# Optimization experiments

Hardware: AMD Instinct MI355X
Metric: run time of the kernel (lower is better)

## Reference

```python
import jax, jax.numpy as jnp
import numpy as np
from jax import lax

BN_EPS = 1e-5
B, C_IN, HW = 512, 3, 128  # crop batch, channels, crop size
C1, C2 = 32, 64
DIST_THRESHOLD = 0.55


def setup_inputs() -> dict:
    key = jax.random.key(0)
    ks = jax.random.split(key, 13)
    return {
        "crops": jax.random.normal(ks[0], (B, C_IN, HW, HW), jnp.float32),
        "w1": jax.random.normal(ks[1], (C1, C_IN, 3, 3), jnp.float32) * 0.1,
        "b1": jax.random.normal(ks[2], (C1,), jnp.float32) * 0.1,
        "g1": jax.random.uniform(ks[3], (C1,), jnp.float32),
        "be1": jax.random.normal(ks[4], (C1,), jnp.float32) * 0.1,
        "m1": jax.random.normal(ks[5], (C1,), jnp.float32) * 0.1,
        "v1": jax.random.uniform(ks[6], (C1,), jnp.float32),
        "w2": jax.random.normal(ks[7], (C2, C1, 3, 3), jnp.float32) * 0.05,
        "b2": jax.random.normal(ks[8], (C2,), jnp.float32) * 0.1,
        "g2": jax.random.uniform(ks[9], (C2,), jnp.float32),
        "be2": jax.random.normal(ks[10], (C2,), jnp.float32) * 0.1,
        "m2": jax.random.normal(ks[11], (C2,), jnp.float32) * 0.1,
        "v2": jax.random.uniform(ks[12], (C2,), jnp.float32),
    }


def _conv(x, w, b, stride):
    y = lax.conv_general_dilated(
        x, w, window_strides=(stride, stride), padding=((1, 1), (1, 1)),
        dimension_numbers=("NCHW", "OIHW", "NCHW"))
    return y + b[None, :, None, None]


def _bn(x, gamma, beta, mean, var):
    inv = gamma * lax.rsqrt(var + BN_EPS)
    return x * inv[None, :, None, None] + (beta - mean * inv)[None, :, None, None]


def _maxpool2(x):
    return lax.reduce_window(x, -jnp.inf, lax.max, (1, 1, 2, 2), (1, 1, 2, 2), "VALID")


def reference(crops, w1, b1, g1, be1, m1, v1, w2, b2, g2, be2, m2, v2):
    # layer1: Conv(3->32, s1, p1) + BN + ReLU + MaxPool2  -> [B, 32, 64, 64]
    h = _maxpool2(jax.nn.relu(_bn(_conv(crops, w1, b1, 1), g1, be1, m1, v1)))
    # layer2: Conv(32->64, s2, p1) + BN + Sigmoid + MaxPool2 -> [B, 64, 16, 16]
    feat = _maxpool2(jax.nn.sigmoid(_bn(_conv(h, w2, b2, 2), g2, be2, m2, v2)))
    # per-crop distribution score thresholded as in uniqueDistribution/MLE
    scores = feat.mean(axis=(1, 2, 3))            # [B]
    detected = scores >= DIST_THRESHOLD           # [B] bool
    return feat, scores, detected
```

## Files before the change

### kernel.cpp

```cpp
#include <hip/hip_runtime.h>
#include <math.h>

#define BN_EPS 1e-5f
#define HW_ 128

typedef unsigned short u16_t;
typedef unsigned int u32_t;

typedef __bf16 bf16x8 __attribute__((ext_vector_type(8)));
typedef float f32x4 __attribute__((ext_vector_type(4)));
typedef float f32x16 __attribute__((ext_vector_type(16)));
typedef u32_t u32x4 __attribute__((ext_vector_type(4)));
typedef u32x4 u32x4_ma __attribute__((may_alias));
typedef u16_t u16_ma __attribute__((may_alias));

static __device__ __forceinline__ u16_t f2bf(float f) {
    u32_t u = __float_as_uint(f);
    return (u16_t)((u + 0x7FFFu + ((u >> 16) & 1u)) >> 16);
}
static __device__ __forceinline__ u32_t packbf(float a, float b) {
    return (u32_t)f2bf(a) | ((u32_t)f2bf(b) << 16);
}
static __device__ __forceinline__ bf16x8 ld_frag16(const u16_t* p) {
    union { u32x4 u; bf16x8 f; } x;
    x.u = *(const u32x4_ma*)p;
    return x.f;
}
static __device__ __forceinline__ bf16x8 ld_frag32(const u32_t* p) {
    union { u32x4 u; bf16x8 f; } x;
    x.u = *(const u32x4_ma*)p;
    return x.f;
}
static __device__ __forceinline__ bf16x8 asbf(u32x4 u) {
    union { u32x4 u; bf16x8 f; } x;
    x.u = u;
    return x.f;
}

#define WSUM_OFF 0
#define W2R_OFF  512
#define WF_OFF   9728
#define PT_OFF   11008
#define BN1_OFF  12288
#define BN2_OFF  12352
#define WS_TOTAL 12480

#define CI_PITCH 304
#define CI_U32   (36 * 152)

__global__ __launch_bounds__(512) void prep_kernel(
    const float* __restrict__ w1, const float* __restrict__ b1,
    const float* __restrict__ g1, const float* __restrict__ be1,
    const float* __restrict__ m1, const float* __restrict__ v1,
    const float* __restrict__ w2, const float* __restrict__ b2,
    const float* __restrict__ g2, const float* __restrict__ be2,
    const float* __restrict__ m2, const float* __restrict__ v2,
    u32_t* __restrict__ ws)
{
    const int tid = threadIdx.x;
    ws[WSUM_OFF + tid] = 0u;

    for (int idx = tid; idx < 9216; idx += 512) {
        int H   = idx / 4608;
        int rem = idx - H * 4608;
        int tap = rem >> 9;
        int r2  = rem & 511;
        int ocl = r2 >> 4;
        int icp = r2 & 15;
        const float* wp = w2 + (H * 32 + ocl) * 288 + tap;
        ws[W2R_OFF + idx] = packbf(wp[(2 * icp) * 9], wp[(2 * icp + 1) * 9]);
    }
    if (tid < 320) {
        int s = tid >> 6, lane = tid & 63;
        int n32 = lane & 31, halfk = lane >> 5;
        int p = 2 * s + halfk;
        bool valid = (p <= 8);
        const float* wp = w1 + n32 * 27 + (valid ? p : 8);
        float wa = valid ? wp[0]  : 0.f;
        float wb = valid ? wp[9]  : 0.f;
        float wc = valid ? wp[18] : 0.f;
        u32x4 f;
        f[0] = packbf(wa, wb); f[1] = packbf(wc, 0.f); f[2] = 0u; f[3] = 0u;
        ((u32x4_ma*)(ws + WF_OFF))[tid] = f;
    }
    for (int idx = tid; idx < 1280; idx += 512) {
        int tt = idx >> 5, n32 = idx & 31;
        int gA = n32 >> 2, sub = n32 & 3;
        int pA = tt * 8 + gA;
        int gy = (pA * 241) >> 12; gy = min(gy, 16);
        int gx = min(pA - gy * 17, 16); gx = max(gx, 0);
        int cy = 2 * gy + (sub >> 1), cx = 2 * gx + (sub & 1);
        ws[PT_OFF + idx] = (u32_t)(cy * CI_PITCH + cx * 8);
    }
    if (tid < 32) {
        float inv = g1[tid] * rsqrtf(v1[tid] + BN_EPS);
        float sh  = b1[tid] * inv + be1[tid] - m1[tid] * inv;
        ws[BN1_OFF + 2 * tid]     = __float_as_uint(inv);
        ws[BN1_OFF + 2 * tid + 1] = __float_as_uint(sh);
    }
    if (tid >= 64 && tid < 128) {
        int ch = tid - 64;
        float inv = g2[ch] * rsqrtf(v2[ch] + BN_EPS);
        float sh  = b2[ch] * inv + be2[ch] - m2[ch] * inv;
        ws[BN2_OFF + 2 * ch]     = __float_as_uint(inv);
        ws[BN2_OFF + 2 * ch + 1] = __float_as_uint(sh);
    }
}

__global__ __launch_bounds__(512, 8) void fused_cnn_kernel(
    const float* __restrict__ crops, const u32_t* __restrict__ tab,
    float* __restrict__ out, float* __restrict__ wsum)
{
    __shared__ __align__(16) u32_t uniS[CI_U32];
    __shared__ __align__(16) u16_t hS[289 * 32];
    __shared__ float redS[8];

    const int tid  = threadIdx.x;
    const int wave = tid >> 6;
    const int lane = tid & 63;
    const int quad = lane >> 4;
    const int r    = lane & 15;
    const int n32  = lane & 31;
    const int halfk = lane >> 5;

    const int blk = blockIdx.x;
    const int img = blk >> 4;
    const int t   = blk & 15;
    const int fy0 = (t >> 2) * 4;
    const int fx0 = (t & 3) * 4;
    const int crop_y0 = 8 * fy0 - 3;
    const int crop_x0 = 8 * fx0 - 3;
    const bool interior = (fy0 != 0) && (fx0 != 0);

    const float* cbase = crops + (size_t)img * (3 * HW_ * HW_);
    #pragma unroll
    for (int i = 0; i < 3; ++i) {
        int idx = tid + 512 * i;
        if (idx < 1296) {
            int rr = (idx * 1821) >> 16;
            int cc = idx - rr * 36;
            int gr = crop_y0 + rr, gc = crop_x0 + cc;
            float v0 = 0.f, v1v = 0.f, v2v = 0.f;
            if (gr >= 0 && gr < HW_ && gc >= 0 && gc < HW_) {
                const float* p = cbase + gr * HW_ + gc;
                v0  = p[0];
                v1v = p[HW_ * HW_];
                v2v = p[2 * HW_ * HW_];
            }
            u32x4 w;
            w[0] = packbf(v0, v1v); w[1] = packbf(v2v, 0.f); w[2] = 0u; w[3] = 0u;
            *(u32x4_ma*)&uniS[rr * 152 + cc * 4] = w;
        }
    }

    u32x4 wf[5];
    const u32x4_ma* wft = (const u32x4_ma*)(tab + WF_OFF);
    #pragma unroll
    for (int s = 0; s < 5; ++s) wf[s] = wft[s * 64 + lane];
    const float inv1 = __uint_as_float(tab[BN1_OFF + 2 * n32]);
    const float sh1  = __uint_as_float(tab[BN1_OFF + 2 * n32 + 1]);
    __syncthreads();

    const int off0 = halfk ? 8          : 0;
    const int off1 = halfk ? 304        : 16;
    const int off2 = halfk ? 304 + 16   : 304 + 8;
    const int off3 = halfk ? 608 + 8    : 608;
    const int off4 = 608 + 16;
    const u16_t* cropsI = (const u16_t*)uniS;
    const int hsub = n32 & 7;
    const int hchk = n32 >> 3;

    #pragma unroll
    for (int i = 0; i < 5; ++i) {
        int tt = wave + 8 * i;
        const u16_t* base = cropsI + tab[PT_OFF + tt * 32 + n32];

        bf16x8 a0 = ld_frag16(base + off0);
        bf16x8 a1 = ld_frag16(base + off1);
        bf16x8 a2 = ld_frag16(base + off2);
        bf16x8 a3 = ld_frag16(base + off3);
        bf16x8 a4 = ld_frag16(base + off4);

        f32x16 acc = {0.f,0.f,0.f,0.f,0.f,0.f,0.f,0.f,
                      0.f,0.f,0.f,0.f,0.f,0.f,0.f,0.f};
        acc = __builtin_amdgcn_mfma_f32_32x32x16_bf16(a0, asbf(wf[0]), acc, 0, 0, 0);
        acc = __builtin_amdgcn_mfma_f32_32x32x16_bf16(a1, asbf(wf[1]), acc, 0, 0, 0);
        acc = __builtin_amdgcn_mfma_f32_32x32x16_bf16(a2, asbf(wf[2]), acc, 0, 0, 0);
        acc = __builtin_amdgcn_mfma_f32_32x32x16_bf16(a3, asbf(wf[3]), acc, 0, 0, 0);
        acc = __builtin_amdgcn_mfma_f32_32x32x16_bf16(a4, asbf(wf[4]), acc, 0, 0, 0);

        #pragma unroll
        for (int q = 0; q < 4; ++q) {
            int pD = tt * 8 + 2 * q + halfk;
            float m4 = fmaxf(fmaxf(acc[4 * q], acc[4 * q + 1]),
                             fmaxf(acc[4 * q + 2], acc[4 * q + 3]));
            float val = fmaxf(fmaf(m4, inv1, sh1), 0.f);
            if (!interior) {
                int gyD = (pD * 241) >> 12;
                int gxD = pD - gyD * 17;
                int y2 = 4 * fy0 - 1 + gyD, x2 = 4 * fx0 - 1 + gxD;
                if (y2 < 0 || y2 > 63 || x2 < 0 || x2 > 63) val = 0.f;
            }
            if (pD < 289) {
                int chk = hchk ^ ((pD >> 1) & 3);
                hS[pD * 32 + chk * 8 + hsub] = f2bf(val);
            }
        }
    }
    __syncthreads();

    float* outp = out + (size_t)img * 16384;
    const f32x4 zero4 = {0.f, 0.f, 0.f, 0.f};
    const int mt  = wave & 1;
    const int nt0 = wave >> 1;
    const int cy2 = 2 * nt0 + ((r >> 1) & 1);
    const int cx2 = 2 * (r >> 2) + (r & 1);
    const int fy  = fy0 + nt0;
    float ssum = 0.f;
    #pragma unroll 1
    for (int H = 0; H < 2; ++H) {
        const u32_t* wz = tab + W2R_OFF + H * 4608;
        const int oc = H * 32 + mt * 16 + r;
        const float s2  = __uint_as_float(tab[BN2_OFF + 2 * oc]);
        const float sh2 = __uint_as_float(tab[BN2_OFF + 2 * oc + 1]);
        f32x4 acc = zero4;
        #pragma unroll
        for (int s = 0; s < 9; ++s) {
            const int ky = s / 3, kx = s - 3 * (s / 3);
            int p = (2 * cy2 + ky) * 17 + (2 * cx2 + kx);
            bf16x8 ah = ld_frag16(&hS[p * 32 + ((quad ^ ((p >> 1) & 3)) << 3)]);
            bf16x8 bw = ld_frag32(&wz[(s * 32 + mt * 16 + r) * 16 + quad * 4]);
            acc = __builtin_amdgcn_mfma_f32_16x16x32_bf16(ah, bw, acc, 0, 0, 0);
        }
        float m4 = fmaxf(fmaxf(acc[0], acc[1]), fmaxf(acc[2], acc[3]));
        float z = fmaf(m4, s2, sh2);
        float sig = 1.f / (1.f + expf(-z));
        outp[oc * 256 + fy * 16 + fx0 + quad] = sig;
        ssum += sig;
    }

    #pragma unroll
    for (int off = 32; off > 0; off >>= 1)
        ssum += __shfl_xor(ssum, off);
    if (lane == 0) redS[wave] = ssum;
    __syncthreads();
    if (tid == 0) {
        float bs = 0.f;
        #pragma unroll
        for (int w = 0; w < 8; ++w) bs += redS[w];
        atomicAdd(&wsum[img], bs);
    }
}

__global__ void finalize_kernel(const float* __restrict__ ws,
                                float* __restrict__ scores,
                                float* __restrict__ detected) {
    int i = threadIdx.x;
    float mean = ws[i] * (1.f / 16384.f);
    scores[i] = mean;
    detected[i] = (mean >= 0.55f) ? 1.f : 0.f;
}

extern "C" void kernel_launch(void* const* d_in, const int* in_sizes, int n_in,
                              void* d_out, int out_size, void* d_ws, size_t ws_size,
                              hipStream_t stream) {
    (void)in_sizes; (void)n_in; (void)out_size; (void)ws_size;
    const float* crops = (const float*)d_in[0];
    const float* w1  = (const float*)d_in[1];
    const float* b1  = (const float*)d_in[2];
    const float* g1  = (const float*)d_in[3];
    const float* be1 = (const float*)d_in[4];
    const float* m1  = (const float*)d_in[5];
    const float* v1  = (const float*)d_in[6];
    const float* w2  = (const float*)d_in[7];
    const float* b2  = (const float*)d_in[8];
    const float* g2  = (const float*)d_in[9];
    const float* be2 = (const float*)d_in[10];
    const float* m2  = (const float*)d_in[11];
    const float* v2  = (const float*)d_in[12];
    float* out = (float*)d_out;
    u32_t* ws  = (u32_t*)d_ws;

    prep_kernel<<<1, 512, 0, stream>>>(
        w1, b1, g1, be1, m1, v1, w2, b2, g2, be2, m2, v2, ws);
    fused_cnn_kernel<<<8192, 512, 0, stream>>>(
        crops, ws, out, (float*)ws);
    finalize_kernel<<<1, 512, 0, stream>>>(
        (const float*)ws, out + 8388608, out + 8388608 + 512);
}
```

Baseline: 289.7 us.

## Repack conv1 input into dense channel-interleaved layout to cut MFMAs from five to three

Changes the shared-memory staging of the input tile from a padded 8-bf16-per-pixel layout to a dense 4-bf16-per-pixel (3 channels plus zero) layout. The conv1 reduction is regrouped so that each 16-wide K slice covers one kernel row, four kx positions times four channels, which needs three MFMAs instead of five. The per-lane pointer table and first-layer weight fragments are rebuilt to match. This lowers LDS footprint, staging stores and matrix-core work for layer 1, at the cost of more 8-byte LDS loads and a larger lookup table.

```diff
diff --git a/kernel.cpp b/kernel.cpp
--- a/kernel.cpp
+++ b/kernel.cpp
@@ -11,8 +11,9 @@
 typedef float f32x4 __attribute__((ext_vector_type(4)));
 typedef float f32x16 __attribute__((ext_vector_type(16)));
 typedef u32_t u32x4 __attribute__((ext_vector_type(4)));
+typedef u32_t u32x2 __attribute__((ext_vector_type(2)));
 typedef u32x4 u32x4_ma __attribute__((may_alias));
-typedef u16_t u16_ma __attribute__((may_alias));
+typedef u32x2 u32x2_ma __attribute__((may_alias));
 
 static __device__ __forceinline__ u16_t f2bf(float f) {
     u32_t u = __float_as_uint(f);
@@ -40,13 +41,12 @@
 #define WSUM_OFF 0
 #define W2R_OFF  512
 #define WF_OFF   9728
-#define PT_OFF   11008
-#define BN1_OFF  12288
-#define BN2_OFF  12352
-#define WS_TOTAL 12480
-
-#define CI_PITCH 304
-#define CI_U32   (36 * 152)
+#define PT_OFF   10496
+#define BN1_OFF  13056
+#define BN2_OFF  13120
+#define WS_TOTAL 13248
+
+#define CI_U32   (36 * 74)
 
 __global__ __launch_bounds__(512) void prep_kernel(
     const float* __restrict__ w1, const float* __restrict__ b1,
@@ -70,27 +70,30 @@
         const float* wp = w2 + (H * 32 + ocl) * 288 + tap;
         ws[W2R_OFF + idx] = packbf(wp[(2 * icp) * 9], wp[(2 * icp + 1) * 9]);
     }
-    if (tid < 320) {
+    if (tid < 192) {
         int s = tid >> 6, lane = tid & 63;
-        int n32 = lane & 31, halfk = lane >> 5;
-        int p = 2 * s + halfk;
-        bool valid = (p <= 8);
-        const float* wp = w1 + n32 * 27 + (valid ? p : 8);
-        float wa = valid ? wp[0]  : 0.f;
-        float wb = valid ? wp[9]  : 0.f;
-        float wc = valid ? wp[18] : 0.f;
+        int n32 = lane & 31, h = lane >> 5;
         u32x4 f;
-        f[0] = packbf(wa, wb); f[1] = packbf(wc, 0.f); f[2] = 0u; f[3] = 0u;
+        #pragma unroll
+        for (int jp = 0; jp < 4; ++jp) {
+            int j0 = 2 * jp, j1 = 2 * jp + 1;
+            int kx0 = 2 * h + (j0 >> 2), ch0 = j0 & 3;
+            int kx1 = 2 * h + (j1 >> 2), ch1 = j1 & 3;
+            float va = (kx0 < 3 && ch0 < 3) ? w1[n32 * 27 + ch0 * 9 + s * 3 + kx0] : 0.f;
+            float vb = (kx1 < 3 && ch1 < 3) ? w1[n32 * 27 + ch1 * 9 + s * 3 + kx1] : 0.f;
+            f[jp] = packbf(va, vb);
+        }
         ((u32x4_ma*)(ws + WF_OFF))[tid] = f;
     }
-    for (int idx = tid; idx < 1280; idx += 512) {
-        int tt = idx >> 5, n32 = idx & 31;
+    for (int idx = tid; idx < 2560; idx += 512) {
+        int tt = idx >> 6, lane = idx & 63;
+        int n32 = lane & 31, h = lane >> 5;
         int gA = n32 >> 2, sub = n32 & 3;
         int pA = tt * 8 + gA;
         int gy = (pA * 241) >> 12; gy = min(gy, 16);
         int gx = min(pA - gy * 17, 16); gx = max(gx, 0);
         int cy = 2 * gy + (sub >> 1), cx = 2 * gx + (sub & 1);
-        ws[PT_OFF + idx] = (u32_t)(cy * CI_PITCH + cx * 8);
+        ws[PT_OFF + idx] = (u32_t)((cy * 37 + cx + 2 * h) * 2);
     }
     if (tid < 32) {
         float inv = g1[tid] * rsqrtf(v1[tid] + BN_EPS);
@@ -136,58 +139,54 @@
     #pragma unroll
     for (int i = 0; i < 3; ++i) {
         int idx = tid + 512 * i;
-        if (idx < 1296) {
-            int rr = (idx * 1821) >> 16;
-            int cc = idx - rr * 36;
+        if (idx < 1332) {
+            int rr = (idx * 1772) >> 16;
+            int cc = idx - rr * 37;
             int gr = crop_y0 + rr, gc = crop_x0 + cc;
             float v0 = 0.f, v1v = 0.f, v2v = 0.f;
-            if (gr >= 0 && gr < HW_ && gc >= 0 && gc < HW_) {
+            if ((unsigned)gr < 128u && (unsigned)gc < 128u) {
                 const float* p = cbase + gr * HW_ + gc;
                 v0  = p[0];
                 v1v = p[HW_ * HW_];
                 v2v = p[2 * HW_ * HW_];
             }
-            u32x4 w;
-            w[0] = packbf(v0, v1v); w[1] = packbf(v2v, 0.f); w[2] = 0u; w[3] = 0u;
-            *(u32x4_ma*)&uniS[rr * 152 + cc * 4] = w;
-        }
-    }
-
-    u32x4 wf[5];
+            u32x2 w;
+            w[0] = packbf(v0, v1v); w[1] = packbf(v2v, 0.f);
+            *(u32x2_ma*)&uniS[idx * 2] = w;
+        }
+    }
+
+    u32x4 wf[3];
     const u32x4_ma* wft = (const u32x4_ma*)(tab + WF_OFF);
     #pragma unroll
-    for (int s = 0; s < 5; ++s) wf[s] = wft[s * 64 + lane];
+    for (int s = 0; s < 3; ++s) wf[s] = wft[s * 64 + lane];
     const float inv1 = __uint_as_float(tab[BN1_OFF + 2 * n32]);
     const float sh1  = __uint_as_float(tab[BN1_OFF + 2 * n32 + 1]);
     __syncthreads();
 
-    const int off0 = halfk ? 8          : 0;
-    const int off1 = halfk ? 304        : 16;
-    const int off2 = halfk ? 304 + 16   : 304 + 8;
-    const int off3 = halfk ? 608 + 8    : 608;
-    const int off4 = 608 + 16;
-    const u16_t* cropsI = (const u16_t*)uniS;
     const int hsub = n32 & 7;
     const int hchk = n32 >> 3;
 
     #pragma unroll
     for (int i = 0; i < 5; ++i) {
         int tt = wave + 8 * i;
-        const u16_t* base = cropsI + tab[PT_OFF + tt * 32 + n32];
-
-        bf16x8 a0 = ld_frag16(base + off0);
-        bf16x8 a1 = ld_frag16(base + off1);
-        bf16x8 a2 = ld_frag16(base + off2);
-        bf16x8 a3 = ld_frag16(base + off3);
-        bf16x8 a4 = ld_frag16(base + off4);
+        const u32_t* bp = uniS + tab[PT_OFF + tt * 64 + lane];
+
+        u32x2 l0a = *(const u32x2_ma*)(bp);
+        u32x2 l0b = *(const u32x2_ma*)(bp + 2);
+        u32x2 l1a = *(const u32x2_ma*)(bp + 74);
+        u32x2 l1b = *(const u32x2_ma*)(bp + 76);
+        u32x2 l2a = *(const u32x2_ma*)(bp + 148);
+        u32x2 l2b = *(const u32x2_ma*)(bp + 150);
+        u32x4 a0; a0[0] = l0a[0]; a0[1] = l0a[1]; a0[2] = l0b[0]; a0[3] = l0b[1];
+        u32x4 a1; a1[0] = l1a[0]; a1[1] = l1a[1]; a1[2] = l1b[0]; a1[3] = l1b[1];
+        u32x4 a2; a2[0] = l2a[0]; a2[1] = l2a[1]; a2[2] = l2b[0]; a2[3] = l2b[1];
 
         f32x16 acc = {0.f,0.f,0.f,0.f,0.f,0.f,0.f,0.f,
                       0.f,0.f,0.f,0.f,0.f,0.f,0.f,0.f};
-        acc = __builtin_amdgcn_mfma_f32_32x32x16_bf16(a0, asbf(wf[0]), acc, 0, 0, 0);
-        acc = __builtin_amdgcn_mfma_f32_32x32x16_bf16(a1, asbf(wf[1]), acc, 0, 0, 0);
-        acc = __builtin_amdgcn_mfma_f32_32x32x16_bf16(a2, asbf(wf[2]), acc, 0, 0, 0);
-        acc = __builtin_amdgcn_mfma_f32_32x32x16_bf16(a3, asbf(wf[3]), acc, 0, 0, 0);
-        acc = __builtin_amdgcn_mfma_f32_32x32x16_bf16(a4, asbf(wf[4]), acc, 0, 0, 0);
+        acc = __builtin_amdgcn_mfma_f32_32x32x16_bf16(asbf(a0), asbf(wf[0]), acc, 0, 0, 0);
+        acc = __builtin_amdgcn_mfma_f32_32x32x16_bf16(asbf(a1), asbf(wf[1]), acc, 0, 0, 0);
+        acc = __builtin_amdgcn_mfma_f32_32x32x16_bf16(asbf(a2), asbf(wf[2]), acc, 0, 0, 0);
 
         #pragma unroll
         for (int q = 0; q < 4; ++q) {
```

After: 286.6 us. Within noise of the previous version (-1.1%).
